# Optimization experiments

Hardware: AMD Instinct MI355X
Metric: run time of the kernel (lower is better)

Reference implementation:

```python
import jax, jax.numpy as jnp
import numpy as np

BSZ, SL, K, D_IN, D_OUT = 2, 1024, 24, 512, 512
K_U, K_Y = 3, 2
USE_HANKEL_L = False


def get_top_eigh(l, k, use_hankel_L):
    i = np.arange(1, l + 1, dtype=np.float64)
    s = i[:, None] + i[None, :]
    if use_hankel_L:
        Z = ((-1.0) ** (s - 2.0) + 1.0) * 8.0 / ((s + 3.0) * (s - 1.0) * (s + 1.0))
    else:
        Z = 2.0 / (s ** 3 - s)
    sigma, phi = np.linalg.eigh(Z)  # ascending
    return jnp.asarray(sigma[-k:], jnp.float32), jnp.asarray(phi[:, -k:], jnp.float32)


def shift(x, k):
    # causal shift along time axis 1, zero-padded at the front
    if k == 0:
        return x
    return jnp.pad(x, ((0, 0), (k, 0), (0, 0)))[:, : x.shape[1]]


def fft_causal_conv(filters, u):
    # filters: (l, k); u: (b, l, d) -> (b, l, k, d) causal convolution per filter
    l = u.shape[1]
    n = 2 * l
    F = jnp.fft.rfft(filters, n=n, axis=0)  # (n//2+1, k)
    U = jnp.fft.rfft(u, n=n, axis=1)        # (b, n//2+1, d)
    Y = jnp.fft.irfft(U[:, :, None, :] * F[None, :, :, None], n=n, axis=1)
    return Y[:, :l].astype(u.dtype)


def compute_ar_u(M_u, u):
    # ar_u[b,t,o] = sum_{i<k_u} M_u[i] @ u_{t-i}
    U = jnp.stack([shift(u, i) for i in range(M_u.shape[0])])  # (k_u, b, l, d_in)
    return jnp.einsum('koi,kbli->blo', M_u, U)


def compute_spectral(u, sigma, phi, M_phi_plus, M_phi_minus, m_y):
    l = u.shape[1]
    phi_s = phi * sigma ** 0.25  # eigenvalue-scaled spectral filters (l, k)
    U_plus = fft_causal_conv(phi_s, u)  # (b, l, k, d_in)
    spec = jnp.einsum('blki,koi->blo', U_plus, M_phi_plus)
    if not USE_HANKEL_L:
        # negative-featurization branch: filters modulated by (-1)^i
        alt = ((-1.0) ** jnp.arange(l)).astype(u.dtype)
        U_minus = fft_causal_conv(phi_s * alt[:, None], u)
        spec = spec + jnp.einsum('blki,koi->blo', U_minus, M_phi_minus)
    if m_y is not None:
        spec = shift(spec, m_y.shape[0])  # spectral features enter at lag k_y (paper: t-2)
    return spec


def compute_ar_y(m_y, y):
    # true short linear recurrence on outputs:
    # yhat_t = y_t + sum_{i=1}^{k_y} m_y[i-1] @ yhat_{t-i}; returns the correction term
    k_y, d_out = m_y.shape[0], m_y.shape[1]
    b = y.shape[0]

    def step(carry, y_t):  # carry: (k_y, b, d_out) = [yhat_{t-1}, ..., yhat_{t-k_y}]
        ar_t = jnp.einsum('koj,kbj->bo', m_y, carry)
        yhat_t = y_t + ar_t
        carry = jnp.concatenate([yhat_t[None], carry[:-1]], axis=0)
        return carry, ar_t

    y_tl = jnp.swapaxes(y, 0, 1)  # (l, b, d_out)
    _, ar = jax.lax.scan(step, jnp.zeros((k_y, b, d_out), y.dtype), y_tl)
    return jnp.swapaxes(ar, 0, 1)


def setup_inputs() -> dict:
    key = jax.random.key(0)
    k0, k1, k2, k3, k4 = jax.random.split(key, 5)
    inputs = jax.random.normal(k0, (BSZ, SL, D_IN), jnp.float32)
    M_u = jax.random.normal(k1, (K_U, D_OUT, D_IN), jnp.float32) * 0.02
    M_phi_plus = jax.random.normal(k2, (K, D_OUT, D_IN), jnp.float32) * 0.02
    M_phi_minus = jax.random.normal(k3, (K, D_OUT, D_IN), jnp.float32) * 0.02
    m_y = jax.random.normal(k4, (K_Y, D_OUT, D_OUT), jnp.float32) * 0.02
    sigma, phi = get_top_eigh(SL, K, USE_HANKEL_L)
    return {'inputs': inputs, 'M_u': M_u, 'M_phi_plus': M_phi_plus,
            'M_phi_minus': M_phi_minus, 'm_y': m_y, 'sigma': sigma, 'phi': phi}


def reference(inputs, M_u, M_phi_plus, M_phi_minus, m_y, sigma, phi):
    ar_u = compute_ar_u(M_u, inputs)
    spectral = compute_spectral(inputs, sigma, phi, M_phi_plus, M_phi_minus, m_y)
    y_t = ar_u + spectral
    y_t = y_t + compute_ar_y(m_y, y_t)  # learnable_m_y=True branch
    return y_t  # dropout p=0.0 (identity)
```

## Files before the change

kernel.cpp:

```cpp
#include <hip/hip_runtime.h>
#include <hip/hip_bf16.h>


typedef unsigned short u16;
typedef __attribute__((ext_vector_type(8))) short  vshort8;
typedef __attribute__((ext_vector_type(4))) short  vshort4;
typedef __attribute__((ext_vector_type(4))) float  f32x4;
typedef __attribute__((ext_vector_type(4))) unsigned int vuint4;

__device__ __forceinline__ u16 f2b(float x) {
  __hip_bfloat16 h = __float2bfloat16(x);
  return __builtin_bit_cast(u16, h);
}
__device__ __forceinline__ float b2f(u16 x) {
  unsigned int u = ((unsigned int)x) << 16;
  return __builtin_bit_cast(float, u);
}

struct GB {
  const u16* A; const u16* B;
  float* Cf; u16* Cb;
  const float* zf; float* out;
  u16* A2T; u16* Au;
  int M, N;
};

template<int V>
__global__ __launch_bounds__(256) void g2(GB a) {
  const int tid = threadIdx.x;
  const int bn = blockIdx.x, bm = blockIdx.y, bz = blockIdx.z;
  const int m0 = bm * 128, n0 = bn * 128;
  __shared__ u16 lA[4096], lB[4096];
  f32x4 acc[4][4];
#pragma unroll
  for (int i = 0; i < 4; i++)
#pragma unroll
    for (int j = 0; j < 4; j++) acc[i][j] = f32x4{0.f, 0.f, 0.f, 0.f};

  int kbeg = 0, kend = 0;
  int cj = 0, cb = 0, cd = 0;
  if (V == 0) kend = 512;
  if (V == 1) { cj = bz & 7; cb = bz >> 3; cd = bm - cj; kend = (cj <= bm) ? 6144 : 0; }
  if (V == 2) {
    int jmax = (m0 >> 6) + 1;
    kbeg = bz * 2048;
    kend = kbeg + 2048;
    int tk = (jmax + 1) * 512;
    if (kend > tk) kend = tk;
    if (kend < kbeg) kend = kbeg;
  }
  if (V == 3) kend = 1024;
  if (V == 5) kend = 1024;

  const int lane = tid & 63, wv = tid >> 6, wr = wv >> 1, wc = wv & 1;
  const u16* Ap = a.A;
  if (V == 5) Ap = a.A + (size_t)bz * 524288;

  for (int k0 = kbeg; k0 < kend; k0 += 32) {
#pragma unroll
    for (int it = 0; it < 2; ++it) {
      int q = tid + it * 256;
      int r = q >> 2, cq = q & 3;
      int kk = k0 + cq * 8;
      vuint4 v;
      if (V == 0) {
        v = *(const vuint4*)(Ap + (size_t)(m0 + r) * 512 + kk);
      } else if (V == 1) {
        v = *(const vuint4*)(Ap + (size_t)cd * 786432 + (size_t)r * 6144 + kk);
      } else if (V == 2) {
        int m = m0 + r, j = m >> 6, b = (m >> 5) & 1, c = m & 31;
        int tau = kk >> 9, p = kk & 511;
        if (tau > j) v = vuint4{0u, 0u, 0u, 0u};
        else v = *(const vuint4*)(Ap + (size_t)(b * 1024 + c * 32 + j - tau) * 512 + p);
      } else if (V == 3) {
        int m = m0 + r;
        if (m < a.M) v = *(const vuint4*)(Ap + (size_t)m * 1024 + kk);
        else v = vuint4{0u, 0u, 0u, 0u};
      } else {
        v = *(const vuint4*)(Ap + (size_t)(m0 + r) * 1024 + kk);
      }
      *(vuint4*)(&lA[(((r >> 4) * 4 + cq) * 16 + (r & 15)) * 8]) = v;

      int n = n0 + r;
      vuint4 w;
      if (V == 0) {
        w = *(const vuint4*)(a.B + (size_t)n * 512 + kk);
      } else if (V == 1) {
        int kh = kk >> 7, sp = kk & 127;
        w = *(const vuint4*)(a.B + (size_t)(cb * 512 + n) * 49152 + kh * 1024 + cj * 128 + sp);
      } else if (V == 2) {
        int tau = kk >> 9, p = kk & 511;
        w = *(const vuint4*)(a.B + (size_t)tau * 524288 + (size_t)n * 1024 + p);
      } else if (V == 3) {
        int jn = n >> 9, o = n & 511;
        w = *(const vuint4*)(a.B + (size_t)(jn + 1) * 524288 + (size_t)o * 1024 + kk);
      } else {
        w = *(const vuint4*)(a.B + (size_t)n * 1024 + kk);
      }
      *(vuint4*)(&lB[(((r >> 4) * 4 + cq) * 16 + (r & 15)) * 8]) = w;
    }
    __syncthreads();
    vshort8 af[4], bf_[4];
#pragma unroll
    for (int s = 0; s < 4; s++) {
      af[s]  = *(const vshort8*)&lA[(((wr * 4 + s) * 4 + (lane >> 4)) * 16 + (lane & 15)) * 8];
      bf_[s] = *(const vshort8*)&lB[(((wc * 4 + s) * 4 + (lane >> 4)) * 16 + (lane & 15)) * 8];
    }
#pragma unroll
    for (int i = 0; i < 4; i++)
#pragma unroll
      for (int j = 0; j < 4; j++)
        acc[i][j] = __builtin_amdgcn_mfma_f32_16x16x32_bf16(af[i], bf_[j], acc[i][j], 0, 0, 0);
    __syncthreads();
  }

#pragma unroll
  for (int i = 0; i < 4; i++) {
    int em = m0 + wr * 64 + i * 16 + ((lane >> 4) << 2);
#pragma unroll
    for (int j = 0; j < 4; j++) {
      int n = n0 + wc * 64 + j * 16 + (lane & 15);
      f32x4 v = acc[i][j];
      if (V == 0) {
        int b = em >> 10, s = em & 1023;
        if (n < 24576) {
          int kh = n >> 9, o = n & 511;
          vshort4 pk = { (short)f2b(v[0]), (short)f2b(v[1]), (short)f2b(v[2]), (short)f2b(v[3]) };
          *(vshort4*)(&a.A2T[(size_t)(b * 512 + o) * 49152 + (size_t)kh * 1024 + s]) = pk;
        } else {
          int jj = (n - 24576) >> 9, o = n & 511;
#pragma unroll
          for (int t = 0; t < 4; t++)
            a.Au[((size_t)(b * 3 + jj) * 1024 + (s + t)) * 512 + o] = f2b(v[t]);
        }
      } else if (V == 1) {
        float* C = a.Cf + (size_t)bz * 524288;
#pragma unroll
        for (int t = 0; t < 4; t++) C[(size_t)(em + t) * 512 + n] = v[t];
      } else if (V == 2) {
        float* C = a.Cf + (size_t)bz * 1048576;
#pragma unroll
        for (int t = 0; t < 4; t++) C[(size_t)(em + t) * 512 + n] = v[t];
      } else if (V == 3) {
        int jj = n >> 9, oo = n & 511;
#pragma unroll
        for (int t = 0; t < 4; t++) {
          int m = em + t;
          if (m < a.M) {
            int b = m >> 5, c = m & 31;
            float zv = a.zf[(size_t)(jj * 64 + b * 32 + c) * 512 + oo];
            a.out[(size_t)b * 524288 + (size_t)(c * 32 + jj) * 512 + oo] = v[t] + zv;
          }
        }
      } else {
        u16* C = a.Cb + (size_t)bz * 524288;
#pragma unroll
        for (int t = 0; t < 4; t++) C[(size_t)(em + t) * 1024 + n] = f2b(v[t]);
      }
    }
  }
}

__global__ void k_prep_X(const float* __restrict__ u, u16* __restrict__ X, int n) {
  int i = blockIdx.x * 256 + threadIdx.x;
  if (i < n) X[i] = f2b(u[i]);
}

__global__ void k_prep_phis(const float* __restrict__ phi, const float* __restrict__ sigma,
                            float* __restrict__ phis) {
  int i = blockIdx.x * 256 + threadIdx.x;
  if (i >= 1024 * 48) return;
  int tau = i / 48, kf = i % 48, k = (kf >= 24) ? kf - 24 : kf;
  float v = phi[tau * 24 + k] * powf(sigma[k], 0.25f);
  if (kf >= 24 && (tau & 1)) v = -v;
  phis[i] = v;
}

__global__ void k_prep_W1(const float* __restrict__ Mp, const float* __restrict__ Mm,
                          const float* __restrict__ Mu, u16* __restrict__ W1) {
  int i = blockIdx.x * 256 + threadIdx.x;
  if (i >= 13369344) return;
  float v;
  if (i < 6291456) v = Mp[i];
  else if (i < 12582912) v = Mm[i - 6291456];
  else v = Mu[i - 12582912];
  W1[i] = f2b(v);
}

__global__ void k_prep_Wtoep(const float* __restrict__ phis, u16* __restrict__ W) {
  int i = blockIdx.x * 256 + threadIdx.x;
  if (i >= 6291456) return;
  int kap = i % 6144, row = i / 6144;
  int tp = row & 127, d = row >> 7;
  int kh = kap >> 7, sp = kap & 127;
  int tau = d * 128 + tp - sp;
  W[i] = (tau >= 0 && tau < 1024) ? f2b(phis[tau * 48 + kh]) : (u16)0;
}

__global__ void k_initTop(const float* __restrict__ my, u16* __restrict__ Top) {
  int i = blockIdx.x * 256 + threadIdx.x;
  if (i >= 1048576) return;
  int mat = i >> 19, rem = i & 524287, o = rem >> 10, k = rem & 1023;
  u16 v;
  if (mat == 0) v = (k == o) ? (u16)0x3F80 : (u16)0;
  else v = (k < 512) ? f2b(my[o * 512 + k]) : f2b(my[262144 + o * 512 + (k - 512)]);
  Top[i] = v;
}

__global__ __launch_bounds__(256) void k_transT(const u16* __restrict__ Top,
                                                u16* __restrict__ STc, int c) {
  __shared__ u16 tile[64][72];
  int tx = blockIdx.x, ty = blockIdx.y;
  int tid = threadIdx.x;
  int r = tid >> 2, seg = tid & 3;
  int k = ty * 64 + r;
  const u16* src = (k < 512) ? Top + (size_t)c * 524288 + (size_t)k * 1024 + tx * 64
                             : Top + (size_t)(c - 1) * 524288 + (size_t)(k - 512) * 1024 + tx * 64;
  *(vuint4*)&tile[r][seg * 16]     = *(const vuint4*)(src + seg * 16);
  *(vuint4*)&tile[r][seg * 16 + 8] = *(const vuint4*)(src + seg * 16 + 8);
  __syncthreads();
  int n = tx * 64 + r;
  u16 tmp[16];
#pragma unroll
  for (int j = 0; j < 16; j++) tmp[j] = tile[seg * 16 + j][r];
  *(vuint4*)&STc[(size_t)n * 1024 + ty * 64 + seg * 16]     = *(vuint4*)&tmp[0];
  *(vuint4*)&STc[(size_t)n * 1024 + ty * 64 + seg * 16 + 8] = *(vuint4*)&tmp[8];
}

__global__ void k_combine(const float* __restrict__ parts, const u16* __restrict__ Au,
                          u16* __restrict__ ybf) {
  int i = blockIdx.x * 256 + threadIdx.x;
  if (i >= 1048576) return;
  int b = i >> 19, rest = i & 524287, t = rest >> 9, o = rest & 511;
  float y = 0.f;
#pragma unroll
  for (int j = 0; j < 3; j++)
    if (t >= j) y += b2f(Au[((size_t)(b * 3 + j) * 1024 + (t - j)) * 512 + o]);
  if (t >= 2) {
    size_t e = (size_t)(t - 2) * 512 + o;
#pragma unroll
    for (int j = 0; j < 8; j++) y += parts[(size_t)(b * 8 + j) * 524288 + e];
  }
  ybf[i] = f2b(y);
}

__global__ void k_zreduce(const float* __restrict__ zp, float* __restrict__ z) {
  int i = blockIdx.x * 256 + threadIdx.x;
  if (i >= 1048576) return;
  float s = 0.f;
#pragma unroll
  for (int j = 0; j < 8; j++) s += zp[(size_t)j * 1048576 + i];
  z[i] = s;
}

__global__ __launch_bounds__(256) void k_bnd(const u16* __restrict__ Top,
                                             const float* __restrict__ zf,
                                             float* __restrict__ bnd,
                                             u16* __restrict__ Abnd, int c) {
  __shared__ float st[2048];
  int tid = threadIdx.x;
  const float* s0 = bnd + (size_t)c * 2048;
  for (int j = tid; j < 2048; j += 256) st[j] = s0[j];
  __syncthreads();
  int q4 = blockIdx.x * 256 + tid;
  int q = q4 >> 2, quarter = q4 & 3;
  int b = q >> 10, kk = q & 1023;
  const u16* row = (kk < 512) ? Top + (size_t)32 * 524288 + (size_t)kk * 1024
                              : Top + (size_t)31 * 524288 + (size_t)(kk - 512) * 1024;
  const float* stb = st + b * 1024 + quarter * 256;
  const u16* rp = row + quarter * 256;
  float sum = 0.f;
  for (int t = 0; t < 32; ++t) {
    vuint4 v = *(const vuint4*)(rp + t * 8);
    const unsigned int* vu = (const unsigned int*)&v;
#pragma unroll
    for (int e = 0; e < 4; ++e) {
      unsigned int pw = vu[e];
      float lo = __builtin_bit_cast(float, (pw & 0xffffu) << 16);
      float hi = __builtin_bit_cast(float, pw & 0xffff0000u);
      sum += lo * stb[t * 8 + e * 2] + hi * stb[t * 8 + e * 2 + 1];
    }
  }
  sum += __shfl_xor(sum, 1);
  sum += __shfl_xor(sum, 2);
  if (quarter == 0) {
    int jrow = (kk < 512) ? 31 : 30, o = kk & 511;
    float s = sum + zf[(size_t)(jrow * 64 + b * 32 + c) * 512 + o];
    bnd[(size_t)(c + 1) * 2048 + b * 1024 + kk] = s;
    Abnd[(size_t)(b * 32 + c + 1) * 1024 + kk] = f2b(s);
  }
}

extern "C" void kernel_launch(void* const* d_in, const int* in_sizes, int n_in,
                              void* d_out, int out_size, void* d_ws, size_t ws_size,
                              hipStream_t stream) {
  const float* u     = (const float*)d_in[0];
  const float* Mu    = (const float*)d_in[1];
  const float* Mp    = (const float*)d_in[2];
  const float* Mm    = (const float*)d_in[3];
  const float* my    = (const float*)d_in[4];
  const float* sigma = (const float*)d_in[5];
  const float* phi   = (const float*)d_in[6];
  float* out = (float*)d_out;

  char* ws = (char*)d_ws;
  size_t off = 0;
  auto alc = [&](size_t b) { size_t p = off; off = (off + b + 255) & ~(size_t)255; return p; };
  u16*  X     = (u16*)(ws + alc(2097152));
  u16*  A2T   = (u16*)(ws + alc(100663296));
  u16*  W1    = (u16*)(ws + alc(26738688));
  u16*  Wtoep = (u16*)(ws + alc(12582912));
  u16*  Au    = (u16*)(ws + alc(6291456));
  float* parts = (float*)(ws + alc(33554432));
  float* phis = (float*)(ws + alc(196608));
  float* bnd  = (float*)(ws + alc(262144));
  u16*  Abnd  = (u16*)(ws + alc(131072));
  if (off > ws_size) return;
  u16*  Top   = W1;
  u16*  STc   = W1 + 17301504;
  u16*  ybf   = A2T;
  float* zf   = (float*)((char*)A2T + 4194304);
  float* zparts = parts;

  k_prep_X<<<dim3(4096), 256, 0, stream>>>(u, X, 1048576);
  k_prep_phis<<<dim3(192), 256, 0, stream>>>(phi, sigma, phis);
  k_prep_W1<<<dim3(52224), 256, 0, stream>>>(Mp, Mm, Mu, W1);
  k_prep_Wtoep<<<dim3(24576), 256, 0, stream>>>(phis, Wtoep);

  {
    GB g{}; g.A = X; g.B = W1; g.A2T = A2T; g.Au = Au; g.M = 2048; g.N = 26112;
    g2<0><<<dim3(204, 16, 1), 256, 0, stream>>>(g);
  }
  {
    GB g{}; g.A = Wtoep; g.B = A2T; g.Cf = parts; g.M = 1024; g.N = 512;
    g2<1><<<dim3(4, 8, 16), 256, 0, stream>>>(g);
  }
  k_combine<<<dim3(4096), 256, 0, stream>>>(parts, Au, ybf);

  k_initTop<<<dim3(4096), 256, 0, stream>>>(my, Top);
  {
    const int cs[5] = {1, 2, 4, 8, 16};
    for (int li = 0; li < 5; ++li) {
      int c = cs[li];
      k_transT<<<dim3(16, 16), 256, 0, stream>>>(Top, STc, c);
      GB s{}; s.A = Top + 524288; s.B = STc; s.Cb = Top + (size_t)(c + 1) * 524288;
      s.M = 512; s.N = 1024;
      g2<5><<<dim3(8, 4, c), 256, 0, stream>>>(s);
    }
  }

  {
    GB g{}; g.A = ybf; g.B = Top; g.Cf = zparts; g.M = 2048; g.N = 512;
    g2<2><<<dim3(4, 16, 8), 256, 0, stream>>>(g);
  }
  k_zreduce<<<dim3(4096), 256, 0, stream>>>(zparts, zf);

  hipMemsetAsync(bnd, 0, 8192, stream);
  hipMemsetAsync(Abnd, 0, 131072, stream);
  for (int c = 0; c < 31; ++c)
    k_bnd<<<dim3(32), 256, 0, stream>>>(Top, zf, bnd, Abnd, c);

  {
    GB g{}; g.A = Abnd; g.B = Top; g.zf = zf; g.out = out; g.M = 64; g.N = 16384;
    g2<3><<<dim3(128, 1, 1), 256, 0, stream>>>(g);
  }
}
```

Baseline: 801.8 us.

## Halve serial boundary recurrence via doubled step matrix; triangular Toeplitz grid

The sequential boundary-state recurrence (31 small dependent launches) becomes a stride-2 recurrence using the squared companion power Top^64. Inputs are precomputed with extra GEMMs (V6), odd states are filled afterward by a batched GEMM (V7), and one more squaring step is added to the power chain. The Toeplitz GEMM grid now launches only lower-triangular blocks with the K dimension split in two, instead of launching idle upper-triangle blocks. The combine kernel sums only the nonzero partials. The workspace is reorganised to fit the larger partial buffer and the extra power matrices. This adds kernels and risks extra bf16 rounding from the higher matrix power.

```diff
diff --git a/kernel.cpp b/kernel.cpp
--- a/kernel.cpp
+++ b/kernel.cpp
@@ -28,7 +28,16 @@
 template<int V>
 __global__ __launch_bounds__(256) void g2(GB a) {
   const int tid = threadIdx.x;
-  const int bn = blockIdx.x, bm = blockIdx.y, bz = blockIdx.z;
+  int bn = blockIdx.x, bm = blockIdx.y;
+  const int bz = blockIdx.z;
+  int cj = 0, cb = 0, cd = 0, chh = 0;
+  if (V == 1) {
+    int p = blockIdx.x;
+    bm = (int)((sqrtf(8.f * (float)p + 1.f) - 1.f) * 0.5f);
+    cj = p - (bm * (bm + 1)) / 2;
+    bn = blockIdx.y;
+    cb = bz >> 1; chh = bz & 1; cd = bm - cj;
+  }
   const int m0 = bm * 128, n0 = bn * 128;
   __shared__ u16 lA[4096], lB[4096];
   f32x4 acc[4][4];
@@ -38,9 +47,8 @@
     for (int j = 0; j < 4; j++) acc[i][j] = f32x4{0.f, 0.f, 0.f, 0.f};
 
   int kbeg = 0, kend = 0;
-  int cj = 0, cb = 0, cd = 0;
   if (V == 0) kend = 512;
-  if (V == 1) { cj = bz & 7; cb = bz >> 3; cd = bm - cj; kend = (cj <= bm) ? 6144 : 0; }
+  if (V == 1) { kbeg = chh * 3072; kend = kbeg + 3072; }
   if (V == 2) {
     int jmax = (m0 >> 6) + 1;
     kbeg = bz * 2048;
@@ -49,8 +57,7 @@
     if (kend > tk) kend = tk;
     if (kend < kbeg) kend = kbeg;
   }
-  if (V == 3) kend = 1024;
-  if (V == 5) kend = 1024;
+  if (V == 3 || V == 5 || V == 6 || V == 7) kend = 1024;
 
   const int lane = tid & 63, wv = tid >> 6, wr = wv >> 1, wc = wv & 1;
   const u16* Ap = a.A;
@@ -76,8 +83,16 @@
         int m = m0 + r;
         if (m < a.M) v = *(const vuint4*)(Ap + (size_t)m * 1024 + kk);
         else v = vuint4{0u, 0u, 0u, 0u};
+      } else if (V == 5) {
+        v = *(const vuint4*)(Ap + (size_t)(m0 + r) * 1024 + kk);
+      } else if (V == 6) {
+        if (r < 64) v = *(const vuint4*)(Ap + (size_t)r * 1024 + kk);
+        else v = vuint4{0u, 0u, 0u, 0u};
       } else {
-        v = *(const vuint4*)(Ap + (size_t)(m0 + r) * 1024 + kk);
+        if (r < 32) {
+          int b = r & 1, k2 = r >> 1;
+          v = *(const vuint4*)(Ap + (size_t)(b * 32 + 2 * k2) * 1024 + kk);
+        } else v = vuint4{0u, 0u, 0u, 0u};
       }
       *(vuint4*)(&lA[(((r >> 4) * 4 + cq) * 16 + (r & 15)) * 8]) = v;
 
@@ -94,8 +109,13 @@
       } else if (V == 3) {
         int jn = n >> 9, o = n & 511;
         w = *(const vuint4*)(a.B + (size_t)(jn + 1) * 524288 + (size_t)o * 1024 + kk);
+      } else if (V == 5) {
+        w = *(const vuint4*)(a.B + (size_t)n * 1024 + kk);
       } else {
-        w = *(const vuint4*)(a.B + (size_t)n * 1024 + kk);
+        const u16* src = (n < 512)
+            ? (a.B + (size_t)32 * 524288 + (size_t)n * 1024 + kk)
+            : (a.B + (size_t)31 * 524288 + (size_t)(n - 512) * 1024 + kk);
+        w = *(const vuint4*)src;
       }
       *(vuint4*)(&lB[(((r >> 4) * 4 + cq) * 16 + (r & 15)) * 8]) = w;
     }
@@ -134,7 +154,7 @@
             a.Au[((size_t)(b * 3 + jj) * 1024 + (s + t)) * 512 + o] = f2b(v[t]);
         }
       } else if (V == 1) {
-        float* C = a.Cf + (size_t)bz * 524288;
+        float* C = a.Cf + (size_t)(cb * 16 + chh * 8 + cj) * 524288;
 #pragma unroll
         for (int t = 0; t < 4; t++) C[(size_t)(em + t) * 512 + n] = v[t];
       } else if (V == 2) {
@@ -152,10 +172,32 @@
             a.out[(size_t)b * 524288 + (size_t)(c * 32 + jj) * 512 + oo] = v[t] + zv;
           }
         }
+      } else if (V == 5) {
+        u16* C = a.Cb + (size_t)bz * 524288;
+#pragma unroll
+        for (int t = 0; t < 4; t++) C[(size_t)(em + t) * 1024 + n] = f2b(v[t]);
+      } else if (V == 6) {
+        int jrow = (n < 512) ? 31 : 30, oo = n & 511;
+#pragma unroll
+        for (int t = 0; t < 4; t++) {
+          int m = em + t;
+          if (m < 62) {
+            int b = m & 1, c = m >> 1;
+            a.Cf[(size_t)m * 1024 + n] =
+                v[t] + a.zf[(size_t)(jrow * 64 + b * 32 + (c + 1)) * 512 + oo];
+          }
+        }
       } else {
-        u16* C = a.Cb + (size_t)bz * 524288;
-#pragma unroll
-        for (int t = 0; t < 4; t++) C[(size_t)(em + t) * 1024 + n] = f2b(v[t]);
+        int jrow = (n < 512) ? 31 : 30, oo = n & 511;
+#pragma unroll
+        for (int t = 0; t < 4; t++) {
+          int m = em + t;
+          if (m < 32) {
+            int b = m & 1, k2 = m >> 1;
+            float val = v[t] + a.zf[(size_t)(jrow * 64 + b * 32 + 2 * k2) * 512 + oo];
+            a.Cb[(size_t)(b * 32 + 2 * k2 + 1) * 1024 + n] = f2b(val);
+          }
+        }
       }
     }
   }
@@ -237,9 +279,11 @@
   for (int j = 0; j < 3; j++)
     if (t >= j) y += b2f(Au[((size_t)(b * 3 + j) * 1024 + (t - j)) * 512 + o]);
   if (t >= 2) {
-    size_t e = (size_t)(t - 2) * 512 + o;
-#pragma unroll
-    for (int j = 0; j < 8; j++) y += parts[(size_t)(b * 8 + j) * 524288 + e];
+    int tp = t - 2, bmv = tp >> 7;
+    size_t e = (size_t)tp * 512 + o;
+    for (int j = 0; j <= bmv; ++j)
+      y += parts[(size_t)(b * 16 + j) * 524288 + e] +
+           parts[(size_t)(b * 16 + 8 + j) * 524288 + e];
   }
   ybf[i] = f2b(y);
 }
@@ -253,20 +297,29 @@
   z[i] = s;
 }
 
-__global__ __launch_bounds__(256) void k_bnd(const u16* __restrict__ Top,
-                                             const float* __restrict__ zf,
-                                             float* __restrict__ bnd,
-                                             u16* __restrict__ Abnd, int c) {
+__global__ void k_wm(const float* __restrict__ zf, u16* __restrict__ Wm) {
+  int i = blockIdx.x * 256 + threadIdx.x;
+  if (i >= 65536) return;
+  int row = i >> 10, n = i & 1023;
+  int b = row & 1, c = row >> 1;
+  int jrow = (n < 512) ? 31 : 30, oo = n & 511;
+  Wm[i] = f2b(zf[(size_t)(jrow * 64 + b * 32 + c) * 512 + oo]);
+}
+
+__global__ __launch_bounds__(256) void k_bnd2(const u16* __restrict__ Top,
+                                              const float* __restrict__ ubuf,
+                                              float* __restrict__ bnd,
+                                              u16* __restrict__ Abnd, int k) {
   __shared__ float st[2048];
   int tid = threadIdx.x;
-  const float* s0 = bnd + (size_t)c * 2048;
+  const float* s0 = bnd + (size_t)k * 2048;
   for (int j = tid; j < 2048; j += 256) st[j] = s0[j];
   __syncthreads();
   int q4 = blockIdx.x * 256 + tid;
   int q = q4 >> 2, quarter = q4 & 3;
   int b = q >> 10, kk = q & 1023;
-  const u16* row = (kk < 512) ? Top + (size_t)32 * 524288 + (size_t)kk * 1024
-                              : Top + (size_t)31 * 524288 + (size_t)(kk - 512) * 1024;
+  const u16* row = (kk < 512) ? Top + (size_t)64 * 524288 + (size_t)kk * 1024
+                              : Top + (size_t)63 * 524288 + (size_t)(kk - 512) * 1024;
   const float* stb = st + b * 1024 + quarter * 256;
   const u16* rp = row + quarter * 256;
   float sum = 0.f;
@@ -284,10 +337,9 @@
   sum += __shfl_xor(sum, 1);
   sum += __shfl_xor(sum, 2);
   if (quarter == 0) {
-    int jrow = (kk < 512) ? 31 : 30, o = kk & 511;
-    float s = sum + zf[(size_t)(jrow * 64 + b * 32 + c) * 512 + o];
-    bnd[(size_t)(c + 1) * 2048 + b * 1024 + kk] = s;
-    Abnd[(size_t)(b * 32 + c + 1) * 1024 + kk] = f2b(s);
+    float s = sum + ubuf[(size_t)(4 * k + b) * 1024 + kk];
+    bnd[(size_t)(k + 1) * 2048 + b * 1024 + kk] = s;
+    Abnd[(size_t)(b * 32 + 2 * k + 2) * 1024 + kk] = f2b(s);
   }
 }
 
@@ -307,20 +359,23 @@
   size_t off = 0;
   auto alc = [&](size_t b) { size_t p = off; off = (off + b + 255) & ~(size_t)255; return p; };
   u16*  X     = (u16*)(ws + alc(2097152));
+  u16*  Wtoep = (u16*)(ws + alc(12582912));
   u16*  A2T   = (u16*)(ws + alc(100663296));
+  u16*  Au    = (u16*)(ws + alc(6291456));
   u16*  W1    = (u16*)(ws + alc(26738688));
-  u16*  Wtoep = (u16*)(ws + alc(12582912));
-  u16*  Au    = (u16*)(ws + alc(6291456));
-  float* parts = (float*)(ws + alc(33554432));
+  char* ptail = ws + alc(40370176); (void)ptail;
   float* phis = (float*)(ws + alc(196608));
-  float* bnd  = (float*)(ws + alc(262144));
+  float* bnd  = (float*)(ws + alc(131072));
   u16*  Abnd  = (u16*)(ws + alc(131072));
+  u16*  Wm    = (u16*)(ws + alc(131072));
+  float* ubuf = (float*)(ws + alc(262144));
   if (off > ws_size) return;
-  u16*  Top   = W1;
-  u16*  STc   = W1 + 17301504;
-  u16*  ybf   = A2T;
-  float* zf   = (float*)((char*)A2T + 4194304);
-  float* zparts = parts;
+  float* partsBig = (float*)W1;
+  float* zparts   = partsBig;
+  u16*  ybf = A2T;
+  float* zf = (float*)((char*)A2T + (4 << 20));
+  u16*  Top = (u16*)((char*)A2T + (size_t)(8 << 20));
+  u16*  STc = (u16*)((char*)A2T + (size_t)(76 << 20));
 
   k_prep_X<<<dim3(4096), 256, 0, stream>>>(u, X, 1048576);
   k_prep_phis<<<dim3(192), 256, 0, stream>>>(phi, sigma, phis);
@@ -332,10 +387,10 @@
     g2<0><<<dim3(204, 16, 1), 256, 0, stream>>>(g);
   }
   {
-    GB g{}; g.A = Wtoep; g.B = A2T; g.Cf = parts; g.M = 1024; g.N = 512;
-    g2<1><<<dim3(4, 8, 16), 256, 0, stream>>>(g);
-  }
-  k_combine<<<dim3(4096), 256, 0, stream>>>(parts, Au, ybf);
+    GB g{}; g.A = Wtoep; g.B = A2T; g.Cf = partsBig; g.M = 1024; g.N = 512;
+    g2<1><<<dim3(36, 4, 4), 256, 0, stream>>>(g);
+  }
+  k_combine<<<dim3(4096), 256, 0, stream>>>(partsBig, Au, ybf);
 
   k_initTop<<<dim3(4096), 256, 0, stream>>>(my, Top);
   {
@@ -347,6 +402,10 @@
       s.M = 512; s.N = 1024;
       g2<5><<<dim3(8, 4, c), 256, 0, stream>>>(s);
     }
+    k_transT<<<dim3(16, 16), 256, 0, stream>>>(Top, STc, 32);
+    GB s{}; s.A = Top + (size_t)31 * 524288; s.B = STc;
+    s.Cb = Top + (size_t)63 * 524288; s.M = 512; s.N = 1024;
+    g2<5><<<dim3(8, 4, 2), 256, 0, stream>>>(s);
   }
 
   {
@@ -355,10 +414,19 @@
   }
   k_zreduce<<<dim3(4096), 256, 0, stream>>>(zparts, zf);
 
+  k_wm<<<dim3(256), 256, 0, stream>>>(zf, Wm);
+  {
+    GB g{}; g.A = Wm; g.B = Top; g.Cf = ubuf; g.zf = zf; g.M = 64; g.N = 1024;
+    g2<6><<<dim3(8, 1, 1), 256, 0, stream>>>(g);
+  }
   hipMemsetAsync(bnd, 0, 8192, stream);
   hipMemsetAsync(Abnd, 0, 131072, stream);
-  for (int c = 0; c < 31; ++c)
-    k_bnd<<<dim3(32), 256, 0, stream>>>(Top, zf, bnd, Abnd, c);
+  for (int k = 0; k < 15; ++k)
+    k_bnd2<<<dim3(32), 256, 0, stream>>>(Top, ubuf, bnd, Abnd, k);
+  {
+    GB g{}; g.A = Abnd; g.B = Top; g.Cb = Abnd; g.zf = zf; g.M = 32; g.N = 1024;
+    g2<7><<<dim3(8, 1, 1), 256, 0, stream>>>(g);
+  }
 
   {
     GB g{}; g.A = Abnd; g.B = Top; g.zf = zf; g.out = out; g.M = 64; g.N = 16384;
```

Result: faster. 779.1 us (-2.8%).
